# Optimization experiments

Hardware: AMD Instinct MI355X
Metric: run time of the kernel (lower is better)

The kernel has to match this reference:

```python
import jax, jax.numpy as jnp
import numpy as np

N_HEAD = 4
TOP_K = 16


def _layernorm(x, g, b, eps=1e-5):
    mu = jnp.mean(x, axis=-1, keepdims=True)
    var = jnp.var(x, axis=-1, keepdims=True)
    return (x - mu) * jax.lax.rsqrt(var + eps) * g + b


def _gelu_new(x):
    c = np.sqrt(2.0 / np.pi).astype(np.float32)
    return 0.5 * x * (1.0 + jnp.tanh(c * (x + 0.044715 * x ** 3)))


def _l2_normalize(x, eps=1e-12):
    n = jnp.sqrt(jnp.sum(x * x, axis=1, keepdims=True))
    return x / jnp.maximum(n, eps)


def setup_inputs() -> dict:
    key = jax.random.key(0)
    ks = jax.random.split(key, 16)
    B, S, DIN, D, L, P, N = 128, 64, 6, 128, 3, 24, 500000
    sd = 0.02
    inp = {
        "x": jax.random.normal(ks[0], (B, S, DIN), jnp.float32),
        "memory_keys": _l2_normalize(jax.random.normal(ks[1], (N, D), jnp.float32)),
        "memory_values": jax.random.normal(ks[2], (N, P, DIN), jnp.float32),
        "wpe": sd * jax.random.normal(ks[3], (S, D), jnp.float32),
        "w_in": sd * jax.random.normal(ks[4], (DIN, D), jnp.float32),
        "b_in": jnp.zeros((D,), jnp.float32),
        "ln1_g": jnp.ones((L, D), jnp.float32),
        "ln1_b": jnp.zeros((L, D), jnp.float32),
        "attn_w": sd * jax.random.normal(ks[5], (L, D, 3 * D), jnp.float32),
        "attn_b": jnp.zeros((L, 3 * D), jnp.float32),
        "attn_pw": sd * jax.random.normal(ks[6], (L, D, D), jnp.float32),
        "attn_pb": jnp.zeros((L, D), jnp.float32),
        "ln2_g": jnp.ones((L, D), jnp.float32),
        "ln2_b": jnp.zeros((L, D), jnp.float32),
        "fc_w": sd * jax.random.normal(ks[7], (L, D, 4 * D), jnp.float32),
        "fc_b": jnp.zeros((L, 4 * D), jnp.float32),
        "mlp_pw": sd * jax.random.normal(ks[8], (L, 4 * D, D), jnp.float32),
        "mlp_pb": jnp.zeros((L, D), jnp.float32),
        "lnf_g": jnp.ones((D,), jnp.float32),
        "lnf_b": jnp.zeros((D,), jnp.float32),
        "w_out": sd * jax.random.normal(ks[9], (S * D, P * DIN), jnp.float32),
        "b_out": jnp.zeros((P * DIN,), jnp.float32),
        "ret_w1": sd * jax.random.normal(ks[10], (DIN, D), jnp.float32),
        "ret_b1": jnp.zeros((D,), jnp.float32),
        "ret_w2": sd * jax.random.normal(ks[11], (S * D, D), jnp.float32),
        "ret_b2": jnp.zeros((D,), jnp.float32),
        "fusion_weight": jnp.float32(0.5),
    }
    return inp


def _forward(x, memory_keys, memory_values, wpe, w_in, b_in, ln1_g, ln1_b,
             attn_w, attn_b, attn_pw, attn_pb, ln2_g, ln2_b, fc_w, fc_b,
             mlp_pw, mlp_pb, lnf_g, lnf_b, w_out, b_out, ret_w1, ret_b1,
             ret_w2, ret_b2, fusion_weight):
    B, S, DIN = x.shape
    D = w_in.shape[1]
    L = attn_w.shape[0]
    P = memory_values.shape[1]
    hd = D // N_HEAD
    # GPT2 backbone with inputs_embeds (eval mode: dropout = identity)
    h = x @ w_in + b_in + wpe[:S]
    causal = jnp.tril(jnp.ones((S, S), bool))
    neg = jnp.finfo(h.dtype).min
    for l in range(L):
        a = _layernorm(h, ln1_g[l], ln1_b[l])
        qkv = a @ attn_w[l] + attn_b[l]                       # [B,S,3D]
        q, k, v = jnp.split(qkv, 3, axis=-1)
        q = q.reshape(B, S, N_HEAD, hd).transpose(0, 2, 1, 3)  # bhsd
        k = k.reshape(B, S, N_HEAD, hd).transpose(0, 2, 1, 3)
        v = v.reshape(B, S, N_HEAD, hd).transpose(0, 2, 1, 3)
        scores = jnp.einsum('bhqd,bhkd->bhqk', q, k) / np.sqrt(hd).astype(np.float32)
        scores = jnp.where(causal, scores, neg)
        att = jax.nn.softmax(scores, axis=-1)
        o = jnp.einsum('bhqk,bhkd->bhqd', att, v)
        o = o.transpose(0, 2, 1, 3).reshape(B, S, D)
        h = h + o @ attn_pw[l] + attn_pb[l]
        m = _layernorm(h, ln2_g[l], ln2_b[l])
        h = h + _gelu_new(m @ fc_w[l] + fc_b[l]) @ mlp_pw[l] + mlp_pb[l]
    h = _layernorm(h, lnf_g, lnf_b)
    base_pred = (h.reshape(B, S * D) @ w_out + b_out).reshape(B, P, DIN)
    # Retrieval branch: encode query, cosine sim against memory, top-k gather
    q_emb = (x @ ret_w1 + ret_b1).reshape(B, S * D) @ ret_w2 + ret_b2
    q_emb = _l2_normalize(q_emb)
    sim = q_emb @ memory_keys.T                               # [B,N] (memory-bound)
    topk_sim, topk_idx = jax.lax.top_k(sim, TOP_K)
    weights = jax.nn.softmax(topk_sim, axis=1)                # [B,K]
    vals = memory_values[topk_idx]                            # [B,K,P,DIN] gather
    retrieved = jnp.einsum('bk,bkpd->bpd', weights, vals)
    alpha = jax.nn.sigmoid(fusion_weight)
    return alpha * base_pred + (1.0 - alpha) * retrieved


def reference(x, memory_keys, memory_values, wpe, w_in, b_in, ln1_g, ln1_b,
              attn_w, attn_b, attn_pw, attn_pb, ln2_g, ln2_b, fc_w, fc_b,
              mlp_pw, mlp_pb, lnf_g, lnf_b, w_out, b_out, ret_w1, ret_b1,
              ret_w2, ret_b2, fusion_weight):
    return _forward(x, memory_keys, memory_values, wpe, w_in, b_in, ln1_g, ln1_b,
                    attn_w, attn_b, attn_pw, attn_pb, ln2_g, ln2_b, fc_w, fc_b,
                    mlp_pw, mlp_pb, lnf_g, lnf_b, w_out, b_out, ret_w1, ret_b1,
                    ret_w2, ret_b2, fusion_weight)
```

## Files before the change

### kernel.cpp

```cpp
#include <hip/hip_runtime.h>
#include <math.h>

#define TOK   8192
#define DM    128
#define NKEY  500000
#define PDIM  144
#define KSPLIT 128

#define SB     256
#define NPASS  7813
#define NCAND  (SB * 16)

typedef __attribute__((ext_vector_type(8))) short short8;
typedef __attribute__((ext_vector_type(4))) float f32x4;

__device__ inline short f2bf(float x) {
    union { float f; unsigned u; } v; v.f = x;
    unsigned r = v.u + 0x7FFFu + ((v.u >> 16) & 1u);
    return (short)(r >> 16);
}
__device__ inline float bf2f(short h) {
    union { float f; unsigned u; } v;
    v.u = ((unsigned)(unsigned short)h) << 16;
    return v.f;
}

__global__ __launch_bounds__(256) void k_embed(
    const float* __restrict__ x, const float* __restrict__ w,
    const float* __restrict__ b, const float* __restrict__ wpe,
    float* __restrict__ out)
{
    int idx = blockIdx.x * 256 + threadIdx.x;
    int t = idx >> 7, d = idx & 127;
    float acc = b[d];
    if (wpe) acc += wpe[(t & 63) * DM + d];
    const float* xr = x + t * 6;
#pragma unroll
    for (int i = 0; i < 6; i++) acc = fmaf(xr[i], w[i * DM + d], acc);
    out[idx] = acc;
}

__global__ __launch_bounds__(256) void k_ln(
    const float* __restrict__ in, const float* __restrict__ g,
    const float* __restrict__ b, float* __restrict__ out)
{
    int row = blockIdx.x * 4 + (threadIdx.x >> 6);
    int lane = threadIdx.x & 63;
    const float* r = in + row * DM;
    float v0 = r[lane], v1 = r[lane + 64];
    float s = v0 + v1, ss = v0 * v0 + v1 * v1;
#pragma unroll
    for (int o = 32; o; o >>= 1) { s += __shfl_down(s, o); ss += __shfl_down(ss, o); }
    s = __shfl(s, 0); ss = __shfl(ss, 0);
    float mean = s * (1.f / 128.f);
    float var = ss * (1.f / 128.f) - mean * mean;
    float rstd = rsqrtf(var + 1e-5f);
    out[row * DM + lane]      = (v0 - mean) * rstd * g[lane]      + b[lane];
    out[row * DM + lane + 64] = (v1 - mean) * rstd * g[lane + 64] + b[lane + 64];
}

template<int KD>
__global__ __launch_bounds__(256) void k_gemm(
    const float* __restrict__ A, const float* __restrict__ W,
    const float* __restrict__ bias, const float* __restrict__ resid,
    float* __restrict__ C, int NC, int act)
{
    __shared__ float As[16][68];
    __shared__ float Ws[16][68];
    const int m0 = blockIdx.x * 64, n0 = blockIdx.y * 64;
    const int tid = threadIdx.x, ty = tid >> 4, tx = tid & 15;
    float acc[4][4];
#pragma unroll
    for (int i = 0; i < 4; i++)
#pragma unroll
        for (int j = 0; j < 4; j++) acc[i][j] = 0.f;

    for (int k0 = 0; k0 < KD; k0 += 16) {
        {
            int m = tid >> 2, kk = (tid & 3) * 4;
            float4 av = *(const float4*)(A + (long)(m0 + m) * KD + k0 + kk);
            As[kk][m] = av.x; As[kk + 1][m] = av.y; As[kk + 2][m] = av.z; As[kk + 3][m] = av.w;
        }
        {
            int kk = tid >> 4, n = (tid & 15) * 4;
            *(float4*)&Ws[kk][n] = *(const float4*)(W + (long)(k0 + kk) * NC + n0 + n);
        }
        __syncthreads();
#pragma unroll
        for (int kk = 0; kk < 16; kk++) {
            float av[4], wv[4];
            *(float4*)av = *(const float4*)&As[kk][ty * 4];
            *(float4*)wv = *(const float4*)&Ws[kk][tx * 4];
#pragma unroll
            for (int i = 0; i < 4; i++)
#pragma unroll
                for (int j = 0; j < 4; j++) acc[i][j] = fmaf(av[i], wv[j], acc[i][j]);
        }
        __syncthreads();
    }
#pragma unroll
    for (int i = 0; i < 4; i++) {
        int m = m0 + ty * 4 + i;
#pragma unroll
        for (int j = 0; j < 4; j++) {
            int n = n0 + tx * 4 + j;
            float v = acc[i][j] + bias[n];
            if (act) {
                float u = v;
                v = 0.5f * u * (1.f + tanhf(0.7978845608028654f * (u + 0.044715f * u * u * u)));
            }
            if (resid) v += resid[(long)m * NC + n];
            C[(long)m * NC + n] = v;
        }
    }
}

__global__ __launch_bounds__(256) void k_attn(
    const float* __restrict__ qkv, float* __restrict__ o)
{
    int b = blockIdx.x >> 2, h = blockIdx.x & 3;
    __shared__ float q[64][33], k[64][33], v[64][33];
    __shared__ float sc[64][65];
    int tid = threadIdx.x;
#pragma unroll
    for (int it = 0; it < 8; it++) {
        int idx = it * 256 + tid; int s = idx >> 5, d = idx & 31;
        const float* base = qkv + (long)(b * 64 + s) * 384 + h * 32 + d;
        q[s][d] = base[0]; k[s][d] = base[128]; v[s][d] = base[256];
    }
    __syncthreads();
    {
        int sq = tid >> 2, sk0 = (tid & 3) * 16;
        for (int j = 0; j < 16; j++) {
            int sk = sk0 + j;
            float acc = 0.f;
#pragma unroll
            for (int d = 0; d < 32; d++) acc = fmaf(q[sq][d], k[sk][d], acc);
            sc[sq][sk] = (sk <= sq) ? acc * 0.17677669529663687f : -3.0e38f;
        }
    }
    __syncthreads();
    if (tid < 64) {
        float m = -3.0e38f;
        for (int j = 0; j < 64; j++) m = fmaxf(m, sc[tid][j]);
        float s = 0.f;
        for (int j = 0; j < 64; j++) { float e = __expf(sc[tid][j] - m); sc[tid][j] = e; s += e; }
        float inv = 1.f / s;
        for (int j = 0; j < 64; j++) sc[tid][j] *= inv;
    }
    __syncthreads();
#pragma unroll
    for (int it = 0; it < 8; it++) {
        int idx = it * 256 + tid; int s = idx >> 5, d = idx & 31;
        float acc = 0.f;
        for (int sk = 0; sk < 64; sk++) acc = fmaf(sc[s][sk], v[sk][d], acc);
        o[(long)(b * 64 + s) * 128 + h * 32 + d] = acc;
    }
}

template<int NC>
__global__ __launch_bounds__(256) void k_head(
    const float* __restrict__ A, const float* __restrict__ W,
    float* __restrict__ part)
{
    constexpr int NPT = NC / 16;
    __shared__ float As[16][132];
    __shared__ float Ws[16][NC + 4];
    const int tid = threadIdx.x, ty = tid >> 4, tx = tid & 15;
    float acc[8][NPT];
#pragma unroll
    for (int i = 0; i < 8; i++)
#pragma unroll
        for (int j = 0; j < NPT; j++) acc[i][j] = 0.f;
    const int kbase = blockIdx.x * 64;
    for (int kc = 0; kc < 4; kc++) {
        int k0 = kbase + kc * 16;
        {
            int m = tid >> 1, kk = (tid & 1) * 8;
            const float* ap = A + (long)m * 8192 + k0 + kk;
            float4 a0 = *(const float4*)ap;
            float4 a1 = *(const float4*)(ap + 4);
            As[kk + 0][m] = a0.x; As[kk + 1][m] = a0.y; As[kk + 2][m] = a0.z; As[kk + 3][m] = a0.w;
            As[kk + 4][m] = a1.x; As[kk + 5][m] = a1.y; As[kk + 6][m] = a1.z; As[kk + 7][m] = a1.w;
        }
        for (int e = tid; e < 16 * NC; e += 256) {
            int kk = e / NC, n = e - kk * NC;
            Ws[kk][n] = W[(long)(k0 + kk) * NC + n];
        }
        __syncthreads();
#pragma unroll
        for (int kk = 0; kk < 16; kk++) {
            float av[8];
            *(float4*)av       = *(const float4*)&As[kk][ty * 8];
            *(float4*)(av + 4) = *(const float4*)&As[kk][ty * 8 + 4];
#pragma unroll
            for (int j = 0; j < NPT; j++) {
                float w = Ws[kk][tx * NPT + j];
#pragma unroll
                for (int i = 0; i < 8; i++) acc[i][j] = fmaf(av[i], w, acc[i][j]);
            }
        }
        __syncthreads();
    }
    float* pp = part + (long)blockIdx.x * (128 * NC);
#pragma unroll
    for (int i = 0; i < 8; i++)
#pragma unroll
        for (int j = 0; j < NPT; j++)
            pp[(ty * 8 + i) * NC + tx * NPT + j] = acc[i][j];
}

__global__ __launch_bounds__(256) void k_redhead(
    const float* __restrict__ part, const float* __restrict__ bias,
    float* __restrict__ out, int MN, int NC)
{
    int idx = blockIdx.x * 256 + threadIdx.x;
    if (idx >= MN) return;
    float s = bias[idx % NC];
    for (int b = 0; b < KSPLIT; b++) s += part[(long)b * MN + idx];
    out[idx] = s;
}

__global__ __launch_bounds__(256) void k_l2norm(float* __restrict__ qe)
{
    int row = blockIdx.x * 4 + (threadIdx.x >> 6);
    int lane = threadIdx.x & 63;
    float v0 = qe[row * 128 + lane], v1 = qe[row * 128 + 64 + lane];
    float ss = v0 * v0 + v1 * v1;
#pragma unroll
    for (int o = 32; o; o >>= 1) ss += __shfl_down(ss, o);
    ss = __shfl(ss, 0);
    float inv = 1.f / fmaxf(sqrtf(ss), 1e-12f);
    qe[row * 128 + lane] = v0 * inv;
    qe[row * 128 + 64 + lane] = v1 * inv;
}

__global__ __launch_bounds__(256) void k_qprep(
    const float* __restrict__ qe, short* __restrict__ qfh, short* __restrict__ qfl)
{
    int idx = blockIdx.x * 256 + threadIdx.x;
    int j = idx & 7, lane = (idx >> 3) & 63, t = (idx >> 9) & 7, ks = idx >> 12;
    int n = t * 16 + (lane & 15);
    int d = ks * 32 + (lane >> 4) * 8 + j;
    float x = qe[n * 128 + d];
    short h = f2bf(x);
    qfh[idx] = h;
    qfl[idx] = f2bf(x - bf2f(h));
}

__global__ __launch_bounds__(512, 2) void k_sim2(
    const float* __restrict__ keys, const short* __restrict__ qfh,
    const short* __restrict__ qfl,
    float* __restrict__ cval, int* __restrict__ cidx)
{
    __shared__ short afh[8192];
    __shared__ short afl[8192];
    __shared__ float sim[8192];
    const int tid = threadIdx.x;
    const int w = tid >> 6, lane = tid & 63;
    const int quad = lane >> 4, l15 = lane & 15;
    const int kg = w >> 2, qg = w & 3;

    short8 bh[4][2], bl[4][2];
    {
        const short8* qfh8 = (const short8*)qfh;
        const short8* qfl8 = (const short8*)qfl;
#pragma unroll
        for (int ks = 0; ks < 4; ks++)
#pragma unroll
            for (int tt = 0; tt < 2; tt++) {
                int f = (ks * 8 + qg * 2 + tt) * 64 + lane;
                bh[ks][tt] = qfh8[f];
                bl[ks][tt] = qfl8[f];
            }
    }

    float tv[16]; int tix[16];
#pragma unroll
    for (int j = 0; j < 16; j++) { tv[j] = -3.0e38f; tix[j] = 0; }
    float runmin = -3.0e38f;

    const int r_loc = tid >> 3;
    const int d0 = (tid & 7) * 16;
    const int mt = r_loc >> 4, rr = r_loc & 15;

    float4 R[4];
    int p = blockIdx.x;
    {
        int gk = p * 64 + r_loc;
#pragma unroll
        for (int c = 0; c < 4; c++) {
            int d = d0 + c * 4;
            R[c] = (gk < NKEY) ? *(const float4*)(keys + (long)gk * 128 + d)
                               : make_float4(0.f, 0.f, 0.f, 0.f);
        }
    }

    for (; p < NPASS; p += SB) {
        __syncthreads();
#pragma unroll
        for (int c = 0; c < 4; c++) {
            int d = d0 + c * 4;
            int ks = d >> 5, qd = (d & 31) >> 3, j = d & 7;
            int slot = (((mt * 4 + ks) * 64) + qd * 16 + rr) * 8 + j;
            float e0 = R[c].x, e1 = R[c].y, e2 = R[c].z, e3 = R[c].w;
            short h0 = f2bf(e0), h1 = f2bf(e1), h2 = f2bf(e2), h3 = f2bf(e3);
            short l0 = f2bf(e0 - bf2f(h0)), l1 = f2bf(e1 - bf2f(h1));
            short l2 = f2bf(e2 - bf2f(h2)), l3 = f2bf(e3 - bf2f(h3));
            int2 hp, lp;
            hp.x = (h0 & 0xFFFF) | ((int)h1 << 16);
            hp.y = (h2 & 0xFFFF) | ((int)h3 << 16);
            lp.x = (l0 & 0xFFFF) | ((int)l1 << 16);
            lp.y = (l2 & 0xFFFF) | ((int)l3 << 16);
            *(int2*)&afh[slot] = hp;
            *(int2*)&afl[slot] = lp;
        }
        {
            int pn = p + SB;
            if (pn < NPASS) {
                int gk = pn * 64 + r_loc;
#pragma unroll
                for (int c = 0; c < 4; c++) {
                    int d = d0 + c * 4;
                    R[c] = (gk < NKEY) ? *(const float4*)(keys + (long)gk * 128 + d)
                                       : make_float4(0.f, 0.f, 0.f, 0.f);
                }
            }
        }
        __syncthreads();

        f32x4 acc[2][2];
#pragma unroll
        for (int m = 0; m < 2; m++)
#pragma unroll
            for (int tt = 0; tt < 2; tt++) acc[m][tt] = (f32x4){0.f, 0.f, 0.f, 0.f};

        const short8* ah8 = (const short8*)afh;
        const short8* al8 = (const short8*)afl;
#pragma unroll
        for (int ks = 0; ks < 4; ks++) {
            short8 a_h[2], a_l[2];
#pragma unroll
            for (int m = 0; m < 2; m++) {
                int f = ((kg * 2 + m) * 4 + ks) * 64 + lane;
                a_h[m] = ah8[f]; a_l[m] = al8[f];
            }
#pragma unroll
            for (int m = 0; m < 2; m++)
#pragma unroll
                for (int tt = 0; tt < 2; tt++) {
                    acc[m][tt] = __builtin_amdgcn_mfma_f32_16x16x32_bf16(a_h[m], bh[ks][tt], acc[m][tt], 0, 0, 0);
                    acc[m][tt] = __builtin_amdgcn_mfma_f32_16x16x32_bf16(a_h[m], bl[ks][tt], acc[m][tt], 0, 0, 0);
                    acc[m][tt] = __builtin_amdgcn_mfma_f32_16x16x32_bf16(a_l[m], bh[ks][tt], acc[m][tt], 0, 0, 0);
                }
        }
        float* sw = sim + w * 1024;
#pragma unroll
        for (int m = 0; m < 2; m++)
#pragma unroll
            for (int tt = 0; tt < 2; tt++)
#pragma unroll
                for (int r = 0; r < 4; r++)
                    sw[(m * 16 + quad * 4 + r) * 32 + tt * 16 + l15] = acc[m][tt][r];
        if (lane < 32) {
            int kbase = p * 64 + kg * 32;
            for (int kk = 0; kk < 32; kk++) {
                int gk2 = kbase + kk;
                float v = sw[kk * 32 + lane];
                if (gk2 < NKEY && v > runmin) {
                    int slot = 0; float mv = tv[0];
#pragma unroll
                    for (int j = 1; j < 16; j++) if (tv[j] < mv) { mv = tv[j]; slot = j; }
                    tv[slot] = v; tix[slot] = gk2;
                    runmin = tv[0];
#pragma unroll
                    for (int j = 1; j < 16; j++) runmin = fminf(runmin, tv[j]);
                }
            }
        }
    }
    __syncthreads();
    float* scv = (float*)afh;
    int*   sci = (int*)afl;
    if (lane < 32) {
        int q = qg * 32 + lane;
#pragma unroll
        for (int j = 0; j < 16; j++) {
            scv[q * 32 + kg * 16 + j] = tv[j];
            sci[q * 32 + kg * 16 + j] = tix[j];
        }
    }
    __syncthreads();
    if (tid < 128) {
        float fv[16]; int fi[16];
#pragma unroll
        for (int j = 0; j < 16; j++) { fv[j] = -3.0e38f; fi[j] = 0; }
        float rm = -3.0e38f;
        for (int e = 0; e < 32; e++) {
            float v = scv[tid * 32 + e];
            if (v > rm) {
                int slot = 0; float mv = fv[0];
#pragma unroll
                for (int j = 1; j < 16; j++) if (fv[j] < mv) { mv = fv[j]; slot = j; }
                fv[slot] = v; fi[slot] = sci[tid * 32 + e];
                rm = fv[0];
#pragma unroll
                for (int j = 1; j < 16; j++) rm = fminf(rm, fv[j]);
            }
        }
        int ob = (blockIdx.x * 128 + tid) * 16;
#pragma unroll
        for (int j = 0; j < 16; j++) { cval[ob + j] = fv[j]; cidx[ob + j] = fi[j]; }
    }
}

__global__ __launch_bounds__(256) void k_merge(
    const float* __restrict__ cval, const int* __restrict__ cidx,
    const float* __restrict__ base, const float* __restrict__ mvals,
    const float* __restrict__ fw, float* __restrict__ out)
{
    __shared__ float sv[NCAND];
    __shared__ int   si[NCAND];
    __shared__ float wv[4]; __shared__ int wi[4];
    __shared__ float tvs[16]; __shared__ int tis[16];
    const int q = blockIdx.x, tid = threadIdx.x;
    for (int i = tid; i < NCAND; i += 256) {
        sv[i] = cval[(i >> 4) * 2048 + q * 16 + (i & 15)];
        si[i] = cidx[(i >> 4) * 2048 + q * 16 + (i & 15)];
    }
    __syncthreads();
    for (int r = 0; r < 16; r++) {
        float bv = -3.0e38f; int bp = -1;
        for (int i = tid; i < NCAND; i += 256) {
            float v = sv[i];
            if (v > bv) { bv = v; bp = i; }
        }
#pragma unroll
        for (int o = 32; o; o >>= 1) {
            float ov = __shfl_down(bv, o); int op = __shfl_down(bp, o);
            if (ov > bv) { bv = ov; bp = op; }
        }
        if ((tid & 63) == 0) { wv[tid >> 6] = bv; wi[tid >> 6] = bp; }
        __syncthreads();
        if (tid == 0) {
            float b2 = wv[0]; int p2 = wi[0];
            for (int ww = 1; ww < 4; ww++) if (wv[ww] > b2) { b2 = wv[ww]; p2 = wi[ww]; }
            tvs[r] = b2; tis[r] = si[p2]; sv[p2] = -3.0e38f;
        }
        __syncthreads();
    }
    float alpha = 1.f / (1.f + expf(-fw[0]));
    if (tid < PDIM) {
        float m = tvs[0];
#pragma unroll
        for (int r = 1; r < 16; r++) m = fmaxf(m, tvs[r]);
        float wgt[16]; float s = 0.f;
#pragma unroll
        for (int r = 0; r < 16; r++) { wgt[r] = expf(tvs[r] - m); s += wgt[r]; }
        float inv = 1.f / s;
        float ret = 0.f;
#pragma unroll
        for (int r = 0; r < 16; r++) ret += wgt[r] * inv * mvals[(long)tis[r] * PDIM + tid];
        out[q * PDIM + tid] = alpha * base[q * PDIM + tid] + (1.f - alpha) * ret;
    }
}

extern "C" void kernel_launch(void* const* d_in, const int* in_sizes, int n_in,
                              void* d_out, int out_size, void* d_ws, size_t ws_size,
                              hipStream_t stream)
{
    const float* x      = (const float*)d_in[0];
    const float* keys   = (const float*)d_in[1];
    const float* mvals  = (const float*)d_in[2];
    const float* wpe    = (const float*)d_in[3];
    const float* w_in   = (const float*)d_in[4];
    const float* b_in   = (const float*)d_in[5];
    const float* ln1_g  = (const float*)d_in[6];
    const float* ln1_b  = (const float*)d_in[7];
    const float* attn_w = (const float*)d_in[8];
    const float* attn_b = (const float*)d_in[9];
    const float* attn_pw= (const float*)d_in[10];
    const float* attn_pb= (const float*)d_in[11];
    const float* ln2_g  = (const float*)d_in[12];
    const float* ln2_b  = (const float*)d_in[13];
    const float* fc_w   = (const float*)d_in[14];
    const float* fc_b   = (const float*)d_in[15];
    const float* mlp_pw = (const float*)d_in[16];
    const float* mlp_pb = (const float*)d_in[17];
    const float* lnf_g  = (const float*)d_in[18];
    const float* lnf_b  = (const float*)d_in[19];
    const float* w_out  = (const float*)d_in[20];
    const float* b_out  = (const float*)d_in[21];
    const float* ret_w1 = (const float*)d_in[22];
    const float* ret_b1 = (const float*)d_in[23];
    const float* ret_w2 = (const float*)d_in[24];
    const float* ret_b2 = (const float*)d_in[25];
    const float* fw     = (const float*)d_in[26];
    float* out = (float*)d_out;

    float* ws   = (float*)d_ws;
    float* h    = ws + 0;
    float* bufA = ws + 1048576;
    float* bufB = ws + 2097152;
    float* bufO = ws + 6291456;
    float* part = ws + 7340032;
    float* base = ws + 9699328;
    float* qe   = ws + 9717760;
    short* qfh  = (short*)(ws + 9734144);
    short* qfl  = (short*)(ws + 9742336);
    float* cval = ws + 9750528;
    int*   cidx = (int*)(ws + 10274816);

    k_embed<<<4096, 256, 0, stream>>>(x, w_in, b_in, wpe, h);
    for (int l = 0; l < 3; l++) {
        k_ln<<<2048, 256, 0, stream>>>(h, ln1_g + l * 128, ln1_b + l * 128, bufA);
        k_gemm<128><<<dim3(128, 6), 256, 0, stream>>>(bufA, attn_w + l * 49152,
            attn_b + l * 384, nullptr, bufB, 384, 0);
        k_attn<<<512, 256, 0, stream>>>(bufB, bufO);
        k_gemm<128><<<dim3(128, 2), 256, 0, stream>>>(bufO, attn_pw + l * 16384,
            attn_pb + l * 128, h, h, 128, 0);
        k_ln<<<2048, 256, 0, stream>>>(h, ln2_g + l * 128, ln2_b + l * 128, bufA);
        k_gemm<128><<<dim3(128, 8), 256, 0, stream>>>(bufA, fc_w + l * 65536,
            fc_b + l * 512, nullptr, bufB, 512, 1);
        k_gemm<512><<<dim3(128, 2), 256, 0, stream>>>(bufB, mlp_pw + l * 65536,
            mlp_pb + l * 128, h, h, 128, 0);
    }
    k_ln<<<2048, 256, 0, stream>>>(h, lnf_g, lnf_b, bufA);
    k_head<144><<<KSPLIT, 256, 0, stream>>>(bufA, w_out, part);
    k_redhead<<<72, 256, 0, stream>>>(part, b_out, base, 128 * 144, 144);

    k_embed<<<4096, 256, 0, stream>>>(x, ret_w1, ret_b1, nullptr, bufO);
    k_head<128><<<KSPLIT, 256, 0, stream>>>(bufO, ret_w2, part);
    k_redhead<<<64, 256, 0, stream>>>(part, ret_b2, qe, 128 * 128, 128);
    k_l2norm<<<32, 256, 0, stream>>>(qe);

    k_qprep<<<64, 256, 0, stream>>>(qe, qfh, qfl);
    k_sim2<<<SB, 512, 0, stream>>>(keys, qfh, qfl, cval, cidx);
    k_merge<<<128, 256, 0, stream>>>(cval, cidx, base, mvals, fw, out);
}
```

Measured before the change: 1.315 ms.

## Fuse layernorm into GEMMs, merge embeds, restructure similarity top-k kernel

Folds LayerNorm into the QKV and FC GEMM prologues and merges the two input embeddings into one launch. It also fuses the L2 norm into the query reduction and qprep, and moves the attention softmax into registers with shuffles. The similarity kernel is rebuilt to use 512 blocks with each wave owning 16 queries across all 64 keys, vectorized bf16 split stores, and a sorted-insertion top-16 with threshold pruning. These changes cut launch count, intermediate global traffic and top-k bookkeeping. The tradeoffs are larger per-block shared memory, a clamped fast-exp GELU, and reuse of workspace buffers for candidates.

```diff
diff --git a/kernel.cpp b/kernel.cpp
--- a/kernel.cpp
+++ b/kernel.cpp
@@ -7,37 +7,61 @@
 #define PDIM  144
 #define KSPLIT 128
 
-#define SB     256
+#define SB     512
 #define NPASS  7813
 #define NCAND  (SB * 16)
 
 typedef __attribute__((ext_vector_type(8))) short short8;
 typedef __attribute__((ext_vector_type(4))) float f32x4;
 
-__device__ inline short f2bf(float x) {
+__device__ __forceinline__ short f2bf(float x) {
     union { float f; unsigned u; } v; v.f = x;
     unsigned r = v.u + 0x7FFFu + ((v.u >> 16) & 1u);
     return (short)(r >> 16);
 }
-__device__ inline float bf2f(short h) {
+__device__ __forceinline__ float bf2f(short h) {
     union { float f; unsigned u; } v;
     v.u = ((unsigned)(unsigned short)h) << 16;
     return v.f;
 }
 
-__global__ __launch_bounds__(256) void k_embed(
+__device__ __forceinline__ void ins16(float v, int id, float* tv, int* tix) {
+#pragma unroll
+    for (int j = 15; j > 0; j--) {
+        bool up = v > tv[j];
+        bool sh = v > tv[j - 1];
+        float nv = sh ? tv[j - 1] : v;
+        int   ni = sh ? tix[j - 1] : id;
+        tv[j]  = up ? nv : tv[j];
+        tix[j] = up ? ni : tix[j];
+    }
+    if (v > tv[0]) { tv[0] = v; tix[0] = id; }
+}
+
+__global__ __launch_bounds__(256) void k_embed2(
     const float* __restrict__ x, const float* __restrict__ w,
     const float* __restrict__ b, const float* __restrict__ wpe,
-    float* __restrict__ out)
-{
-    int idx = blockIdx.x * 256 + threadIdx.x;
-    int t = idx >> 7, d = idx & 127;
-    float acc = b[d];
-    if (wpe) acc += wpe[(t & 63) * DM + d];
-    const float* xr = x + t * 6;
-#pragma unroll
-    for (int i = 0; i < 6; i++) acc = fmaf(xr[i], w[i * DM + d], acc);
-    out[idx] = acc;
+    float* __restrict__ out, const float* __restrict__ rw,
+    const float* __restrict__ rb, float* __restrict__ rout)
+{
+    int bid = blockIdx.x;
+    if (bid < 4096) {
+        int idx = bid * 256 + threadIdx.x;
+        int t = idx >> 7, d = idx & 127;
+        float acc = b[d] + wpe[(t & 63) * DM + d];
+        const float* xr = x + t * 6;
+#pragma unroll
+        for (int i = 0; i < 6; i++) acc = fmaf(xr[i], w[i * DM + d], acc);
+        out[idx] = acc;
+    } else {
+        int idx = (bid - 4096) * 256 + threadIdx.x;
+        int t = idx >> 7, d = idx & 127;
+        float acc = rb[d];
+        const float* xr = x + t * 6;
+#pragma unroll
+        for (int i = 0; i < 6; i++) acc = fmaf(xr[i], rw[i * DM + d], acc);
+        rout[idx] = acc;
+    }
 }
 
 __global__ __launch_bounds__(256) void k_ln(
@@ -59,11 +83,87 @@
     out[row * DM + lane + 64] = (v1 - mean) * rstd * g[lane + 64] + b[lane + 64];
 }
 
+template<int ACT>
+__global__ __launch_bounds__(256) void k_gemmln(
+    const float* __restrict__ A, const float* __restrict__ g,
+    const float* __restrict__ bln, const float* __restrict__ W,
+    const float* __restrict__ bias, float* __restrict__ C, int NC)
+{
+    __shared__ float As[128][68];
+    __shared__ float Ws[16][68];
+    const int tid = threadIdx.x;
+    const int m0 = blockIdx.x * 64, n0 = blockIdx.y * 64;
+    {
+        int row = tid >> 2, part = tid & 3;
+        const float* ar = A + (long)(m0 + row) * 128 + part * 32;
+        float v[32];
+        float s = 0.f, ss = 0.f;
+#pragma unroll
+        for (int i2 = 0; i2 < 8; i2++) {
+            float4 t = *(const float4*)(ar + i2 * 4);
+            v[i2 * 4 + 0] = t.x; v[i2 * 4 + 1] = t.y;
+            v[i2 * 4 + 2] = t.z; v[i2 * 4 + 3] = t.w;
+            s += t.x + t.y + t.z + t.w;
+            ss += t.x * t.x + t.y * t.y + t.z * t.z + t.w * t.w;
+        }
+        s += __shfl_xor(s, 1); s += __shfl_xor(s, 2);
+        ss += __shfl_xor(ss, 1); ss += __shfl_xor(ss, 2);
+        float mean = s * (1.f / 128.f);
+        float rstd = rsqrtf(ss * (1.f / 128.f) - mean * mean + 1e-5f);
+#pragma unroll
+        for (int i = 0; i < 32; i++) {
+            int d = part * 32 + i;
+            As[d][row] = (v[i] - mean) * rstd * g[d] + bln[d];
+        }
+    }
+    const int ty = tid >> 4, tx = tid & 15;
+    float acc[4][4];
+#pragma unroll
+    for (int i = 0; i < 4; i++)
+#pragma unroll
+        for (int j = 0; j < 4; j++) acc[i][j] = 0.f;
+    __syncthreads();
+    for (int k0 = 0; k0 < 128; k0 += 16) {
+        {
+            int kk = tid >> 4, n = (tid & 15) * 4;
+            *(float4*)&Ws[kk][n] = *(const float4*)(W + (long)(k0 + kk) * NC + n0 + n);
+        }
+        __syncthreads();
+#pragma unroll
+        for (int kk = 0; kk < 16; kk++) {
+            float av[4], wv[4];
+            *(float4*)av = *(const float4*)&As[k0 + kk][ty * 4];
+            *(float4*)wv = *(const float4*)&Ws[kk][tx * 4];
+#pragma unroll
+            for (int i = 0; i < 4; i++)
+#pragma unroll
+                for (int j = 0; j < 4; j++) acc[i][j] = fmaf(av[i], wv[j], acc[i][j]);
+        }
+        __syncthreads();
+    }
+#pragma unroll
+    for (int i = 0; i < 4; i++) {
+        int m = m0 + ty * 4 + i;
+#pragma unroll
+        for (int j = 0; j < 4; j++) {
+            int n = n0 + tx * 4 + j;
+            float u = acc[i][j] + bias[n];
+            if (ACT) {
+                float z = 0.7978845608028654f * (u + 0.044715f * u * u * u);
+                z = fminf(fmaxf(z, -15.f), 15.f);
+                float t = __expf(2.f * z);
+                u = 0.5f * u * (1.f + (t - 1.f) / (t + 1.f));
+            }
+            C[(long)m * NC + n] = u;
+        }
+    }
+}
+
 template<int KD>
 __global__ __launch_bounds__(256) void k_gemm(
     const float* __restrict__ A, const float* __restrict__ W,
     const float* __restrict__ bias, const float* __restrict__ resid,
-    float* __restrict__ C, int NC, int act)
+    float* __restrict__ C, int NC)
 {
     __shared__ float As[16][68];
     __shared__ float Ws[16][68];
@@ -74,7 +174,6 @@
     for (int i = 0; i < 4; i++)
 #pragma unroll
         for (int j = 0; j < 4; j++) acc[i][j] = 0.f;
-
     for (int k0 = 0; k0 < KD; k0 += 16) {
         {
             int m = tid >> 2, kk = (tid & 3) * 4;
@@ -104,13 +203,9 @@
 #pragma unroll
         for (int j = 0; j < 4; j++) {
             int n = n0 + tx * 4 + j;
-            float v = acc[i][j] + bias[n];
-            if (act) {
-                float u = v;
-                v = 0.5f * u * (1.f + tanhf(0.7978845608028654f * (u + 0.044715f * u * u * u)));
-            }
-            if (resid) v += resid[(long)m * NC + n];
-            C[(long)m * NC + n] = v;
+            float u = acc[i][j] + bias[n];
+            if (resid) u += resid[(long)m * NC + n];
+            C[(long)m * NC + n] = u;
         }
     }
 }
@@ -120,7 +215,7 @@
 {
     int b = blockIdx.x >> 2, h = blockIdx.x & 3;
     __shared__ float q[64][33], k[64][33], v[64][33];
-    __shared__ float sc[64][65];
+    __shared__ float att[64][65];
     int tid = threadIdx.x;
 #pragma unroll
     for (int it = 0; it < 8; it++) {
@@ -131,29 +226,31 @@
     __syncthreads();
     {
         int sq = tid >> 2, sk0 = (tid & 3) * 16;
+        float e[16]; float mx = -3.0e38f;
+#pragma unroll
         for (int j = 0; j < 16; j++) {
             int sk = sk0 + j;
-            float acc = 0.f;
-#pragma unroll
-            for (int d = 0; d < 32; d++) acc = fmaf(q[sq][d], k[sk][d], acc);
-            sc[sq][sk] = (sk <= sq) ? acc * 0.17677669529663687f : -3.0e38f;
-        }
-    }
-    __syncthreads();
-    if (tid < 64) {
-        float m = -3.0e38f;
-        for (int j = 0; j < 64; j++) m = fmaxf(m, sc[tid][j]);
+            float a = 0.f;
+#pragma unroll
+            for (int d = 0; d < 32; d++) a = fmaf(q[sq][d], k[sk][d], a);
+            a = (sk <= sq) ? a * 0.17677669529663687f : -3.0e38f;
+            e[j] = a; mx = fmaxf(mx, a);
+        }
+        mx = fmaxf(mx, __shfl_xor(mx, 1)); mx = fmaxf(mx, __shfl_xor(mx, 2));
         float s = 0.f;
-        for (int j = 0; j < 64; j++) { float e = __expf(sc[tid][j] - m); sc[tid][j] = e; s += e; }
+#pragma unroll
+        for (int j = 0; j < 16; j++) { e[j] = __expf(e[j] - mx); s += e[j]; }
+        s += __shfl_xor(s, 1); s += __shfl_xor(s, 2);
         float inv = 1.f / s;
-        for (int j = 0; j < 64; j++) sc[tid][j] *= inv;
+#pragma unroll
+        for (int j = 0; j < 16; j++) att[sq][sk0 + j] = e[j] * inv;
     }
     __syncthreads();
 #pragma unroll
     for (int it = 0; it < 8; it++) {
         int idx = it * 256 + tid; int s = idx >> 5, d = idx & 31;
         float acc = 0.f;
-        for (int sk = 0; sk < 64; sk++) acc = fmaf(sc[s][sk], v[sk][d], acc);
+        for (int sk = 0; sk < 64; sk++) acc = fmaf(att[s][sk], v[sk][d], acc);
         o[(long)(b * 64 + s) * 128 + h * 32 + d] = acc;
     }
 }
@@ -195,9 +292,9 @@
             *(float4*)(av + 4) = *(const float4*)&As[kk][ty * 8 + 4];
 #pragma unroll
             for (int j = 0; j < NPT; j++) {
-                float w = Ws[kk][tx * NPT + j];
-#pragma unroll
-                for (int i = 0; i < 8; i++) acc[i][j] = fmaf(av[i], w, acc[i][j]);
+                float wv = Ws[kk][tx * NPT + j];
+#pragma unroll
+                for (int i = 0; i < 8; i++) acc[i][j] = fmaf(av[i], wv, acc[i][j]);
             }
         }
         __syncthreads();
@@ -221,173 +318,190 @@
     out[idx] = s;
 }
 
-__global__ __launch_bounds__(256) void k_l2norm(float* __restrict__ qe)
-{
-    int row = blockIdx.x * 4 + (threadIdx.x >> 6);
-    int lane = threadIdx.x & 63;
-    float v0 = qe[row * 128 + lane], v1 = qe[row * 128 + 64 + lane];
-    float ss = v0 * v0 + v1 * v1;
-#pragma unroll
-    for (int o = 32; o; o >>= 1) ss += __shfl_down(ss, o);
-    ss = __shfl(ss, 0);
-    float inv = 1.f / fmaxf(sqrtf(ss), 1e-12f);
-    qe[row * 128 + lane] = v0 * inv;
-    qe[row * 128 + 64 + lane] = v1 * inv;
+__global__ __launch_bounds__(256) void k_redhead_qe(
+    const float* __restrict__ part, const float* __restrict__ bias,
+    float* __restrict__ out, float* __restrict__ ssq)
+{
+    __shared__ float hsum[4];
+    int tid = threadIdx.x;
+    int idx = blockIdx.x * 256 + tid;
+    float s = bias[idx & 127];
+    for (int b = 0; b < KSPLIT; b++) s += part[(long)b * 16384 + idx];
+    out[idx] = s;
+    float sq = s * s;
+#pragma unroll
+    for (int o = 32; o; o >>= 1) sq += __shfl_down(sq, o);
+    if ((tid & 63) == 0) hsum[tid >> 6] = sq;
+    __syncthreads();
+    if (tid == 0)   ssq[blockIdx.x * 2]     = hsum[0] + hsum[1];
+    if (tid == 128) ssq[blockIdx.x * 2 + 1] = hsum[2] + hsum[3];
 }
 
 __global__ __launch_bounds__(256) void k_qprep(
-    const float* __restrict__ qe, short* __restrict__ qfh, short* __restrict__ qfl)
+    const float* __restrict__ qe, const float* __restrict__ ssq,
+    short* __restrict__ qfh, short* __restrict__ qfl)
 {
     int idx = blockIdx.x * 256 + threadIdx.x;
     int j = idx & 7, lane = (idx >> 3) & 63, t = (idx >> 9) & 7, ks = idx >> 12;
     int n = t * 16 + (lane & 15);
     int d = ks * 32 + (lane >> 4) * 8 + j;
-    float x = qe[n * 128 + d];
+    float inv = 1.f / fmaxf(sqrtf(ssq[n]), 1e-12f);
+    float x = qe[n * 128 + d] * inv;
     short h = f2bf(x);
     qfh[idx] = h;
     qfl[idx] = f2bf(x - bf2f(h));
 }
 
-__global__ __launch_bounds__(512, 2) void k_sim2(
+__device__ __forceinline__ void cvt8(float4 a, float4 b, int4& hi, int4& lo) {
+    float e[8] = {a.x, a.y, a.z, a.w, b.x, b.y, b.z, b.w};
+    int h[8], l[8];
+#pragma unroll
+    for (int i = 0; i < 8; i++) {
+        short hh = f2bf(e[i]);
+        h[i] = (int)hh & 0xFFFF;
+        l[i] = (int)f2bf(e[i] - bf2f(hh)) & 0xFFFF;
+    }
+    hi.x = h[0] | (h[1] << 16); hi.y = h[2] | (h[3] << 16);
+    hi.z = h[4] | (h[5] << 16); hi.w = h[6] | (h[7] << 16);
+    lo.x = l[0] | (l[1] << 16); lo.y = l[2] | (l[3] << 16);
+    lo.z = l[4] | (l[5] << 16); lo.w = l[6] | (l[7] << 16);
+}
+
+__global__ __launch_bounds__(512, 2) void k_sim3(
     const float* __restrict__ keys, const short* __restrict__ qfh,
     const short* __restrict__ qfl,
     float* __restrict__ cval, int* __restrict__ cidx)
 {
-    __shared__ short afh[8192];
-    __shared__ short afl[8192];
-    __shared__ float sim[8192];
+    __shared__ __align__(16) char sm[67584];
+    short* afh = (short*)sm;
+    short* afl = (short*)(sm + 16384);
+    float* simb = (float*)(sm + 32768);
+
     const int tid = threadIdx.x;
     const int w = tid >> 6, lane = tid & 63;
     const int quad = lane >> 4, l15 = lane & 15;
-    const int kg = w >> 2, qg = w & 3;
-
-    short8 bh[4][2], bl[4][2];
+    const int qg = w;
+
+    short8 bh[4], bl[4];
     {
         const short8* qfh8 = (const short8*)qfh;
         const short8* qfl8 = (const short8*)qfl;
 #pragma unroll
-        for (int ks = 0; ks < 4; ks++)
-#pragma unroll
-            for (int tt = 0; tt < 2; tt++) {
-                int f = (ks * 8 + qg * 2 + tt) * 64 + lane;
-                bh[ks][tt] = qfh8[f];
-                bl[ks][tt] = qfl8[f];
-            }
+        for (int ks = 0; ks < 4; ks++) {
+            int f = (ks * 8 + qg) * 64 + lane;
+            bh[ks] = qfh8[f]; bl[ks] = qfl8[f];
+        }
     }
 
     float tv[16]; int tix[16];
 #pragma unroll
     for (int j = 0; j < 16; j++) { tv[j] = -3.0e38f; tix[j] = 0; }
-    float runmin = -3.0e38f;
-
-    const int r_loc = tid >> 3;
-    const int d0 = (tid & 7) * 16;
-    const int mt = r_loc >> 4, rr = r_loc & 15;
+
+    const int r = tid >> 3, o = tid & 7;
+    const int mt = r >> 4, rr = r & 15;
+    const int L = (o & 3) * 16 + rr;
+    const int t8a = mt * 4 + (o >> 2);
+    const int t8b = mt * 4 + 2 + (o >> 2);
+    short* dha = afh + (t8a * 64 + L) * 8;
+    short* dla = afl + (t8a * 64 + L) * 8;
+    short* dhb = afh + (t8b * 64 + L) * 8;
+    short* dlb = afl + (t8b * 64 + L) * 8;
+
+    const int q_own = l15, kq = quad;
+    float* sw = simb + w * 1088;
 
     float4 R[4];
     int p = blockIdx.x;
     {
-        int gk = p * 64 + r_loc;
-#pragma unroll
-        for (int c = 0; c < 4; c++) {
-            int d = d0 + c * 4;
-            R[c] = (gk < NKEY) ? *(const float4*)(keys + (long)gk * 128 + d)
-                               : make_float4(0.f, 0.f, 0.f, 0.f);
-        }
+        int gk = p * 64 + r;
+        const float* kp = keys + (long)gk * 128 + o * 8;
+        bool ok = gk < NKEY;
+        R[0] = ok ? *(const float4*)kp        : make_float4(0.f,0.f,0.f,0.f);
+        R[1] = ok ? *(const float4*)(kp + 4)  : make_float4(0.f,0.f,0.f,0.f);
+        R[2] = ok ? *(const float4*)(kp + 64) : make_float4(0.f,0.f,0.f,0.f);
+        R[3] = ok ? *(const float4*)(kp + 68) : make_float4(0.f,0.f,0.f,0.f);
     }
 
     for (; p < NPASS; p += SB) {
-        __syncthreads();
-#pragma unroll
-        for (int c = 0; c < 4; c++) {
-            int d = d0 + c * 4;
-            int ks = d >> 5, qd = (d & 31) >> 3, j = d & 7;
-            int slot = (((mt * 4 + ks) * 64) + qd * 16 + rr) * 8 + j;
-            float e0 = R[c].x, e1 = R[c].y, e2 = R[c].z, e3 = R[c].w;
-            short h0 = f2bf(e0), h1 = f2bf(e1), h2 = f2bf(e2), h3 = f2bf(e3);
-            short l0 = f2bf(e0 - bf2f(h0)), l1 = f2bf(e1 - bf2f(h1));
-            short l2 = f2bf(e2 - bf2f(h2)), l3 = f2bf(e3 - bf2f(h3));
-            int2 hp, lp;
-            hp.x = (h0 & 0xFFFF) | ((int)h1 << 16);
-            hp.y = (h2 & 0xFFFF) | ((int)h3 << 16);
-            lp.x = (l0 & 0xFFFF) | ((int)l1 << 16);
-            lp.y = (l2 & 0xFFFF) | ((int)l3 << 16);
-            *(int2*)&afh[slot] = hp;
-            *(int2*)&afl[slot] = lp;
+        {
+            int4 hi, lo;
+            cvt8(R[0], R[1], hi, lo);
+            *(int4*)dha = hi; *(int4*)dla = lo;
+            cvt8(R[2], R[3], hi, lo);
+            *(int4*)dhb = hi; *(int4*)dlb = lo;
         }
         {
             int pn = p + SB;
             if (pn < NPASS) {
-                int gk = pn * 64 + r_loc;
-#pragma unroll
-                for (int c = 0; c < 4; c++) {
-                    int d = d0 + c * 4;
-                    R[c] = (gk < NKEY) ? *(const float4*)(keys + (long)gk * 128 + d)
-                                       : make_float4(0.f, 0.f, 0.f, 0.f);
-                }
+                int gk = pn * 64 + r;
+                const float* kp = keys + (long)gk * 128 + o * 8;
+                bool ok = gk < NKEY;
+                R[0] = ok ? *(const float4*)kp        : make_float4(0.f,0.f,0.f,0.f);
+                R[1] = ok ? *(const float4*)(kp + 4)  : make_float4(0.f,0.f,0.f,0.f);
+                R[2] = ok ? *(const float4*)(kp + 64) : make_float4(0.f,0.f,0.f,0.f);
+                R[3] = ok ? *(const float4*)(kp + 68) : make_float4(0.f,0.f,0.f,0.f);
             }
         }
         __syncthreads();
 
-        f32x4 acc[2][2];
-#pragma unroll
-        for (int m = 0; m < 2; m++)
-#pragma unroll
-            for (int tt = 0; tt < 2; tt++) acc[m][tt] = (f32x4){0.f, 0.f, 0.f, 0.f};
-
+        f32x4 acc[4];
+#pragma unroll
+        for (int m = 0; m < 4; m++) acc[m] = (f32x4){0.f, 0.f, 0.f, 0.f};
         const short8* ah8 = (const short8*)afh;
         const short8* al8 = (const short8*)afl;
 #pragma unroll
         for (int ks = 0; ks < 4; ks++) {
-            short8 a_h[2], a_l[2];
-#pragma unroll
-            for (int m = 0; m < 2; m++) {
-                int f = ((kg * 2 + m) * 4 + ks) * 64 + lane;
-                a_h[m] = ah8[f]; a_l[m] = al8[f];
+            short8 ah[4], al[4];
+#pragma unroll
+            for (int m = 0; m < 4; m++) {
+                int f = (m * 4 + ks) * 64 + lane;
+                ah[m] = ah8[f]; al[m] = al8[f];
             }
 #pragma unroll
-            for (int m = 0; m < 2; m++)
-#pragma unroll
-                for (int tt = 0; tt < 2; tt++) {
-                    acc[m][tt] = __builtin_amdgcn_mfma_f32_16x16x32_bf16(a_h[m], bh[ks][tt], acc[m][tt], 0, 0, 0);
-                    acc[m][tt] = __builtin_amdgcn_mfma_f32_16x16x32_bf16(a_h[m], bl[ks][tt], acc[m][tt], 0, 0, 0);
-                    acc[m][tt] = __builtin_amdgcn_mfma_f32_16x16x32_bf16(a_l[m], bh[ks][tt], acc[m][tt], 0, 0, 0);
-                }
-        }
-        float* sw = sim + w * 1024;
-#pragma unroll
-        for (int m = 0; m < 2; m++)
-#pragma unroll
-            for (int tt = 0; tt < 2; tt++)
-#pragma unroll
-                for (int r = 0; r < 4; r++)
-                    sw[(m * 16 + quad * 4 + r) * 32 + tt * 16 + l15] = acc[m][tt][r];
-        if (lane < 32) {
-            int kbase = p * 64 + kg * 32;
-            for (int kk = 0; kk < 32; kk++) {
-                int gk2 = kbase + kk;
-                float v = sw[kk * 32 + lane];
-                if (gk2 < NKEY && v > runmin) {
-                    int slot = 0; float mv = tv[0];
-#pragma unroll
-                    for (int j = 1; j < 16; j++) if (tv[j] < mv) { mv = tv[j]; slot = j; }
-                    tv[slot] = v; tix[slot] = gk2;
-                    runmin = tv[0];
-#pragma unroll
-                    for (int j = 1; j < 16; j++) runmin = fminf(runmin, tv[j]);
-                }
+            for (int m = 0; m < 4; m++) {
+                acc[m] = __builtin_amdgcn_mfma_f32_16x16x32_bf16(ah[m], bh[ks], acc[m], 0, 0, 0);
+                acc[m] = __builtin_amdgcn_mfma_f32_16x16x32_bf16(ah[m], bl[ks], acc[m], 0, 0, 0);
+                acc[m] = __builtin_amdgcn_mfma_f32_16x16x32_bf16(al[m], bh[ks], acc[m], 0, 0, 0);
             }
         }
-    }
+#pragma unroll
+        for (int m = 0; m < 4; m++)
+#pragma unroll
+            for (int r4 = 0; r4 < 4; r4++)
+                sw[(m * 16 + quad * 4 + r4) * 17 + l15] = acc[m][r4];
+        __syncthreads();
+
+        int limit = NKEY - p * 64;
+        float thr = tv[15];
+#pragma unroll
+        for (int bb = 0; bb < 2; bb++) {
+            float vv[8];
+#pragma unroll
+            for (int i = 0; i < 8; i++) {
+                int kk = kq * 16 + bb * 8 + i;
+                float vx = sw[kk * 17 + q_own];
+                vv[i] = (kk < limit) ? vx : -3.0e38f;
+            }
+            float mx = fmaxf(fmaxf(fmaxf(vv[0], vv[1]), fmaxf(vv[2], vv[3])),
+                             fmaxf(fmaxf(vv[4], vv[5]), fmaxf(vv[6], vv[7])));
+            if (mx > thr) {
+                int kb = p * 64 + kq * 16 + bb * 8;
+#pragma unroll
+                for (int i = 0; i < 8; i++)
+                    if (vv[i] > thr) { ins16(vv[i], kb + i, tv, tix); thr = tv[15]; }
+            }
+        }
+    }
+
     __syncthreads();
-    float* scv = (float*)afh;
-    int*   sci = (int*)afl;
-    if (lane < 32) {
-        int q = qg * 32 + lane;
+    float* scv = (float*)sm;
+    int*   sci = (int*)(sm + 32768);
+    {
+        int q = qg * 16 + q_own;
 #pragma unroll
         for (int j = 0; j < 16; j++) {
-            scv[q * 32 + kg * 16 + j] = tv[j];
-            sci[q * 32 + kg * 16 + j] = tix[j];
+            scv[q * 64 + kq * 16 + j] = tv[j];
+            sci[q * 64 + kq * 16 + j] = tix[j];
         }
     }
     __syncthreads();
@@ -395,18 +509,9 @@
         float fv[16]; int fi[16];
 #pragma unroll
         for (int j = 0; j < 16; j++) { fv[j] = -3.0e38f; fi[j] = 0; }
-        float rm = -3.0e38f;
-        for (int e = 0; e < 32; e++) {
-            float v = scv[tid * 32 + e];
-            if (v > rm) {
-                int slot = 0; float mv = fv[0];
-#pragma unroll
-                for (int j = 1; j < 16; j++) if (fv[j] < mv) { mv = fv[j]; slot = j; }
-                fv[slot] = v; fi[slot] = sci[tid * 32 + e];
-                rm = fv[0];
-#pragma unroll
-                for (int j = 1; j < 16; j++) rm = fminf(rm, fv[j]);
-            }
+        for (int e = 0; e < 64; e++) {
+            float vx = scv[tid * 64 + e];
+            if (vx > fv[15]) ins16(vx, sci[tid * 64 + e], fv, fi);
         }
         int ob = (blockIdx.x * 128 + tid) * 16;
 #pragma unroll
@@ -449,14 +554,14 @@
         }
         __syncthreads();
     }
-    float alpha = 1.f / (1.f + expf(-fw[0]));
+    float alpha = 1.f / (1.f + __expf(-fw[0]));
     if (tid < PDIM) {
         float m = tvs[0];
 #pragma unroll
         for (int r = 1; r < 16; r++) m = fmaxf(m, tvs[r]);
         float wgt[16]; float s = 0.f;
 #pragma unroll
-        for (int r = 0; r < 16; r++) { wgt[r] = expf(tvs[r] - m); s += wgt[r]; }
+        for (int r = 0; r < 16; r++) { wgt[r] = __expf(tvs[r] - m); s += wgt[r]; }
         float inv = 1.f / s;
         float ret = 0.f;
 #pragma unroll
@@ -506,35 +611,32 @@
     float* part = ws + 7340032;
     float* base = ws + 9699328;
     float* qe   = ws + 9717760;
-    short* qfh  = (short*)(ws + 9734144);
-    short* qfl  = (short*)(ws + 9742336);
-    float* cval = ws + 9750528;
-    int*   cidx = (int*)(ws + 10274816);
-
-    k_embed<<<4096, 256, 0, stream>>>(x, w_in, b_in, wpe, h);
+    float* ssq  = ws + 9734144;
+    short* qfh  = (short*)(ws + 9734272);
+    short* qfl  = (short*)(ws + 9742464);
+    float* cval = bufB;
+    int*   cidx = (int*)part;
+
+    k_embed2<<<8192, 256, 0, stream>>>(x, w_in, b_in, wpe, h, ret_w1, ret_b1, bufO);
     for (int l = 0; l < 3; l++) {
-        k_ln<<<2048, 256, 0, stream>>>(h, ln1_g + l * 128, ln1_b + l * 128, bufA);
-        k_gemm<128><<<dim3(128, 6), 256, 0, stream>>>(bufA, attn_w + l * 49152,
-            attn_b + l * 384, nullptr, bufB, 384, 0);
-        k_attn<<<512, 256, 0, stream>>>(bufB, bufO);
-        k_gemm<128><<<dim3(128, 2), 256, 0, stream>>>(bufO, attn_pw + l * 16384,
-            attn_pb + l * 128, h, h, 128, 0);
-        k_ln<<<2048, 256, 0, stream>>>(h, ln2_g + l * 128, ln2_b + l * 128, bufA);
-        k_gemm<128><<<dim3(128, 8), 256, 0, stream>>>(bufA, fc_w + l * 65536,
-            fc_b + l * 512, nullptr, bufB, 512, 1);
+        k_gemmln<0><<<dim3(128, 6), 256, 0, stream>>>(h, ln1_g + l * 128,
+            ln1_b + l * 128, attn_w + l * 49152, attn_b + l * 384, bufB, 384);
+        k_attn<<<512, 256, 0, stream>>>(bufB, bufA);
+        k_gemm<128><<<dim3(128, 2), 256, 0, stream>>>(bufA, attn_pw + l * 16384,
+            attn_pb + l * 128, h, h, 128);
+        k_gemmln<1><<<dim3(128, 8), 256, 0, stream>>>(h, ln2_g + l * 128,
+            ln2_b + l * 128, fc_w + l * 65536, fc_b + l * 512, bufB, 512);
         k_gemm<512><<<dim3(128, 2), 256, 0, stream>>>(bufB, mlp_pw + l * 65536,
-            mlp_pb + l * 128, h, h, 128, 0);
+            mlp_pb + l * 128, h, h, 128);
     }
     k_ln<<<2048, 256, 0, stream>>>(h, lnf_g, lnf_b, bufA);
     k_head<144><<<KSPLIT, 256, 0, stream>>>(bufA, w_out, part);
     k_redhead<<<72, 256, 0, stream>>>(part, b_out, base, 128 * 144, 144);
 
-    k_embed<<<4096, 256, 0, stream>>>(x, ret_w1, ret_b1, nullptr, bufO);
     k_head<128><<<KSPLIT, 256, 0, stream>>>(bufO, ret_w2, part);
-    k_redhead<<<64, 256, 0, stream>>>(part, ret_b2, qe, 128 * 128, 128);
-    k_l2norm<<<32, 256, 0, stream>>>(qe);
-
-    k_qprep<<<64, 256, 0, stream>>>(qe, qfh, qfl);
-    k_sim2<<<SB, 512, 0, stream>>>(keys, qfh, qfl, cval, cidx);
+    k_redhead_qe<<<64, 256, 0, stream>>>(part, ret_b2, qe, ssq);
+    k_qprep<<<64, 256, 0, stream>>>(qe, ssq, qfh, qfl);
+
+    k_sim3<<<SB, 512, 0, stream>>>(keys, qfh, qfl, cval, cidx);
     k_merge<<<128, 256, 0, stream>>>(cval, cidx, base, mvals, fw, out);
 }
```

Result: faster. 1.237 ms (-5.9%).
